# Kernel tuning notes

Hardware: AMD Instinct MI355X
Metric: run time of the kernel (lower is better)

The kernel has to match this reference:

```python
import jax, jax.numpy as jnp
import numpy as np

N = 100000       # num nodes
E = 3200000      # num edges (avg degree 32)
F_IN = 128       # num_node_features
HID = 16         # hidden dim hard-coded in Net
C = 10           # num_classes


def setup_inputs() -> dict:
    key = jax.random.key(0)
    k1, k2, k3, k4 = jax.random.split(key, 4)
    x = jax.random.normal(k1, (N, F_IN), dtype=jnp.float32)
    edge_index = jax.random.randint(k2, (2, E), 0, N, dtype=jnp.int32)
    W1 = jax.random.normal(k3, (F_IN, HID), dtype=jnp.float32) * 0.05
    b1 = jnp.zeros((HID,), dtype=jnp.float32)
    W2 = jax.random.normal(k4, (HID, C), dtype=jnp.float32) * 0.05
    b2 = jnp.zeros((C,), dtype=jnp.float32)
    return {"x": x, "edge_index": edge_index, "W1": W1, "b1": b1, "W2": W2, "b2": b2}


def reference(x, edge_index, W1, b1, W2, b2):
    # GCNConv: out = D^{-1/2} (A + I) D^{-1/2} X W + b   (add self-loops)
    loops = jnp.arange(N, dtype=edge_index.dtype)
    row = jnp.concatenate([edge_index[0], loops])  # source nodes
    col = jnp.concatenate([edge_index[1], loops])  # target nodes

    # symmetric normalization (degrees include self-loops, so deg >= 1)
    deg = jax.ops.segment_sum(jnp.ones_like(col, dtype=jnp.float32), col, num_segments=N)
    dis = jax.lax.rsqrt(deg)
    norm = dis[row] * dis[col]  # [E+N]

    def gcn_conv(h, W, b):
        h = h @ W                               # [N, d_out] small GEMM first
        msg = h[row] * norm[:, None]            # gather + scale, [E+N, d_out]
        out = jax.ops.segment_sum(msg, col, num_segments=N)  # scatter-add
        return out + b

    h = jax.nn.relu(gcn_conv(x, W1, b1))
    # F.dropout(training=False) is identity in eval mode
    logits = gcn_conv(h, W2, b2)
    return jax.nn.log_softmax(logits, axis=1)
```

## Files before the change

kernel.cpp:

```cpp
#include <hip/hip_runtime.h>
#include <math.h>

#define N_NODES 100000
#define N_EDGES 3200000
#define F_IN 128
#define HID 16
#define C_OUT 10
#define WIN 256
#define NDIG 391
#define PNB2 500
#define EPB 6400
#define SCN (NDIG * PNB2)
#define SB1 764
#define MAXE 40

typedef unsigned short u16;
typedef unsigned int u32;

__device__ __forceinline__ float bf2f(u16 u) {
    return __uint_as_float(((u32)u) << 16);
}
__device__ __forceinline__ u16 f2bf(float f) {
    u32 x = __float_as_uint(f);
    u32 r = (x + 0x7fffu + ((x >> 16) & 1u)) >> 16;
    return (u16)r;
}
__device__ __forceinline__ void acc8(float* a, uint4 w) {
    a[0] += bf2f((u16)(w.x & 0xffff)); a[1] += bf2f((u16)(w.x >> 16));
    a[2] += bf2f((u16)(w.y & 0xffff)); a[3] += bf2f((u16)(w.y >> 16));
    a[4] += bf2f((u16)(w.z & 0xffff)); a[5] += bf2f((u16)(w.z >> 16));
    a[6] += bf2f((u16)(w.w & 0xffff)); a[7] += bf2f((u16)(w.w >> 16));
}

__global__ void k_pcnt(const int* __restrict__ col, int* __restrict__ blkhistA) {
    __shared__ int h[NDIG];
    for (int i = threadIdx.x; i < NDIG; i += 256) h[i] = 0;
    __syncthreads();
    const uint4* c4 = (const uint4*)(col + blockIdx.x * EPB);
    for (int i = threadIdx.x; i < EPB / 4; i += 256) {
        uint4 c = c4[i];
        atomicAdd(&h[c.x >> 8], 1);
        atomicAdd(&h[c.y >> 8], 1);
        atomicAdd(&h[c.z >> 8], 1);
        atomicAdd(&h[c.w >> 8], 1);
    }
    __syncthreads();
    for (int d = threadIdx.x; d < NDIG; d += 256)
        blkhistA[d * PNB2 + blockIdx.x] = h[d];
}

__global__ void k_s1(const int* __restrict__ blkhistA, int* __restrict__ psum) {
    __shared__ int sm[256];
    int i = blockIdx.x * 256 + threadIdx.x;
    sm[threadIdx.x] = (i < SCN) ? blkhistA[i] : 0;
    __syncthreads();
    for (int off = 128; off > 0; off >>= 1) {
        if (threadIdx.x < off) sm[threadIdx.x] += sm[threadIdx.x + off];
        __syncthreads();
    }
    if (threadIdx.x == 0) psum[blockIdx.x] = sm[0];
}

__global__ void k_s2(int* __restrict__ psum) {
    const int T = 1024;
    __shared__ int part[T];
    int t = threadIdx.x;
    int v0 = (t < SB1) ? psum[t] : 0;
    part[t] = v0;
    __syncthreads();
    for (int off = 1; off < T; off <<= 1) {
        int v = part[t];
        int u = (t >= off) ? part[t - off] : 0;
        __syncthreads();
        part[t] = v + u;
        __syncthreads();
    }
    if (t < SB1) psum[t] = part[t] - v0;
}

__global__ void k_s3(const int* __restrict__ blkhistA, const int* __restrict__ psum,
                     int* __restrict__ blkhistB) {
    __shared__ int sm[256];
    int i = blockIdx.x * 256 + threadIdx.x;
    int t = threadIdx.x;
    int v = (i < SCN) ? blkhistA[i] : 0;
    sm[t] = v;
    __syncthreads();
    for (int off = 1; off < 256; off <<= 1) {
        int a = sm[t];
        int b = (t >= off) ? sm[t - off] : 0;
        __syncthreads();
        sm[t] = a + b;
        __syncthreads();
    }
    if (i < SCN) blkhistB[i] = psum[blockIdx.x] + sm[t] - v;
}

__global__ void __launch_bounds__(512) k_pwrite(
        const int* __restrict__ row, const int* __restrict__ col,
        const int* __restrict__ blkhistA, const int* __restrict__ blkhistB,
        u32* __restrict__ staging) {
    __shared__ u32 sorted[EPB];
    __shared__ u16 dwin[EPB];
    __shared__ int gbase[NDIG];
    __shared__ int lbase[NDIG];
    __shared__ int lcur[NDIG];
    __shared__ int scan[512];

    int t = threadIdx.x;
    int b = blockIdx.x;
    int hv = 0;
    if (t < NDIG) {
        hv = blkhistA[t * PNB2 + b];
        gbase[t] = blkhistB[t * PNB2 + b];
        lcur[t] = 0;
    }
    scan[t] = hv;
    __syncthreads();
    for (int off = 1; off < 512; off <<= 1) {
        int v = scan[t];
        int u = (t >= off) ? scan[t - off] : 0;
        __syncthreads();
        scan[t] = v + u;
        __syncthreads();
    }
    if (t < NDIG) lbase[t] = scan[t] - hv;
    __syncthreads();

    const uint4* c4 = (const uint4*)(col + b * EPB);
    const uint4* r4 = (const uint4*)(row + b * EPB);
    for (int i = t; i < EPB / 4; i += 512) {
        uint4 c = c4[i];
        uint4 r = r4[i];
        int d, rank, pos;
        d = (int)(c.x >> 8); rank = atomicAdd(&lcur[d], 1); pos = lbase[d] + rank;
        sorted[pos] = ((c.x & 255u) << 17) | r.x; dwin[pos] = (u16)d;
        d = (int)(c.y >> 8); rank = atomicAdd(&lcur[d], 1); pos = lbase[d] + rank;
        sorted[pos] = ((c.y & 255u) << 17) | r.y; dwin[pos] = (u16)d;
        d = (int)(c.z >> 8); rank = atomicAdd(&lcur[d], 1); pos = lbase[d] + rank;
        sorted[pos] = ((c.z & 255u) << 17) | r.z; dwin[pos] = (u16)d;
        d = (int)(c.w >> 8); rank = atomicAdd(&lcur[d], 1); pos = lbase[d] + rank;
        sorted[pos] = ((c.w & 255u) << 17) | r.w; dwin[pos] = (u16)d;
    }
    __syncthreads();

    for (int i = t; i < EPB; i += 512) {
        int d = dwin[i];
        staging[gbase[d] + (i - lbase[d])] = sorted[i];
    }
}

__global__ void k_csr(u32* staging, const int* __restrict__ blkhistB,
                      int* __restrict__ offs, float* __restrict__ dis) {
    __shared__ int cnt[WIN];
    __shared__ int base[WIN];
    int w = blockIdx.x;
    int t = threadIdx.x;
    cnt[t] = 0;
    __syncthreads();
    int start = blkhistB[w * PNB2];
    int end = (w == NDIG - 1) ? N_EDGES : blkhistB[(w + 1) * PNB2];
    u32 buf[MAXE];
    int n = 0;
#pragma unroll
    for (int k = 0; k < MAXE; k++) {
        int i = start + k * 256 + t;
        if (i < end) {
            u32 e = staging[i];
            buf[k] = e;
            n = k + 1;
            atomicAdd(&cnt[e >> 17], 1);
        }
    }
    __syncthreads();
    base[t] = cnt[t];
    __syncthreads();
    for (int off = 1; off < WIN; off <<= 1) {
        int v = base[t];
        int u = (t >= off) ? base[t - off] : 0;
        __syncthreads();
        base[t] = v + u;
        __syncthreads();
    }
    int excl = base[t] - cnt[t];
    base[t] = excl;
    int node = w * WIN + t;
    if (node < N_NODES) {
        offs[node] = start + excl;
        dis[node] = rsqrtf(1.0f + (float)cnt[t]);
    }
    if (w == 0 && t == 0) offs[N_NODES] = N_EDGES;
    __syncthreads();
    cnt[t] = 0;
    __syncthreads();
#pragma unroll
    for (int k = 0; k < MAXE; k++) {
        if (k < n) {
            u32 e = buf[k];
            int cl = (int)(e >> 17);
            int rank = atomicAdd(&cnt[cl], 1);
            staging[start + base[cl] + rank] = e;
        }
    }
}

__global__ void k_gemm1(const float* __restrict__ x, const float* __restrict__ W1,
                        const float* __restrict__ dis, u16* __restrict__ h1s) {
    __shared__ float Ws[F_IN * HID];
    for (int t = threadIdx.x; t < F_IN * HID; t += blockDim.x) Ws[t] = W1[t];
    __syncthreads();

    int node = blockIdx.x * blockDim.x + threadIdx.x;
    if (node >= N_NODES) return;

    float acc[HID];
#pragma unroll
    for (int j = 0; j < HID; j++) acc[j] = 0.f;

    const float4* xr = (const float4*)(x + (size_t)node * F_IN);
#pragma unroll 2
    for (int k4 = 0; k4 < F_IN / 4; k4++) {
        float4 v = xr[k4];
        float xv[4] = {v.x, v.y, v.z, v.w};
#pragma unroll
        for (int kk = 0; kk < 4; kk++) {
            const float4* wr = (const float4*)(Ws + (k4 * 4 + kk) * HID);
            float4 w0 = wr[0], w1 = wr[1], w2 = wr[2], w3 = wr[3];
            float xs = xv[kk];
            acc[0]  += xs * w0.x; acc[1]  += xs * w0.y; acc[2]  += xs * w0.z; acc[3]  += xs * w0.w;
            acc[4]  += xs * w1.x; acc[5]  += xs * w1.y; acc[6]  += xs * w1.z; acc[7]  += xs * w1.w;
            acc[8]  += xs * w2.x; acc[9]  += xs * w2.y; acc[10] += xs * w2.z; acc[11] += xs * w2.w;
            acc[12] += xs * w3.x; acc[13] += xs * w3.y; acc[14] += xs * w3.z; acc[15] += xs * w3.w;
        }
    }

    float d = dis[node];
    u32 p[8];
#pragma unroll
    for (int i = 0; i < 8; i++)
        p[i] = (u32)f2bf(acc[2 * i] * d) | ((u32)f2bf(acc[2 * i + 1] * d) << 16);
    u32* dst = (u32*)(h1s + (size_t)node * HID);
#pragma unroll
    for (int i = 0; i < 8; i++) dst[i] = p[i];
}

__global__ void k_gather1(const int* __restrict__ offs, const u32* __restrict__ csr,
                          const float* __restrict__ dis, const u16* __restrict__ h1s,
                          u16* __restrict__ agg1) {
    int t = blockIdx.x * 256 + threadIdx.x;
    if (t >= N_NODES * 2) return;
    int node = t >> 1;
    int half = t & 1;
    const uint4* hb = (const uint4*)h1s;
    float a[8] = {0.f, 0.f, 0.f, 0.f, 0.f, 0.f, 0.f, 0.f};
    acc8(a, hb[(size_t)node * 2 + half]);
    int s0 = offs[node], s1 = offs[node + 1];
    int j = s0;
    for (; j < s1 && (j & 3); j++)
        acc8(a, hb[(size_t)(csr[j] & 0x1FFFFu) * 2 + half]);
    for (; j + 4 <= s1; j += 4) {
        uint4 ss = *(const uint4*)(csr + j);
        uint4 w0 = hb[(size_t)(ss.x & 0x1FFFFu) * 2 + half];
        uint4 w1 = hb[(size_t)(ss.y & 0x1FFFFu) * 2 + half];
        uint4 w2 = hb[(size_t)(ss.z & 0x1FFFFu) * 2 + half];
        uint4 w3 = hb[(size_t)(ss.w & 0x1FFFFu) * 2 + half];
        acc8(a, w0); acc8(a, w1); acc8(a, w2); acc8(a, w3);
    }
    for (; j < s1; j++)
        acc8(a, hb[(size_t)(csr[j] & 0x1FFFFu) * 2 + half]);
    float dc = dis[node];
    uint4 o;
    o.x = (u32)f2bf(a[0] * dc) | ((u32)f2bf(a[1] * dc) << 16);
    o.y = (u32)f2bf(a[2] * dc) | ((u32)f2bf(a[3] * dc) << 16);
    o.z = (u32)f2bf(a[4] * dc) | ((u32)f2bf(a[5] * dc) << 16);
    o.w = (u32)f2bf(a[6] * dc) | ((u32)f2bf(a[7] * dc) << 16);
    ((uint4*)agg1)[(size_t)node * 2 + half] = o;
}

__global__ void k_layer2(const u16* __restrict__ agg1, const float* __restrict__ b1,
                         const float* __restrict__ W2, const float* __restrict__ dis,
                         u16* __restrict__ h2s) {
    __shared__ float Ws[HID * C_OUT];
    __shared__ float b1s[HID];
    if (threadIdx.x < HID * C_OUT) Ws[threadIdx.x] = W2[threadIdx.x];
    if (threadIdx.x < HID) b1s[threadIdx.x] = b1[threadIdx.x];
    __syncthreads();

    int node = blockIdx.x * blockDim.x + threadIdx.x;
    if (node >= N_NODES) return;

    const uint4* ar = (const uint4*)(agg1 + (size_t)node * HID);
    uint4 q0 = ar[0], q1 = ar[1];
    u32 qs[8] = {q0.x, q0.y, q0.z, q0.w, q1.x, q1.y, q1.z, q1.w};

    float acc[C_OUT];
#pragma unroll
    for (int k = 0; k < C_OUT; k++) acc[k] = 0.f;

#pragma unroll
    for (int i = 0; i < 8; i++) {
        u32 q = qs[i];
        float v0 = bf2f((u16)(q & 0xffff));
        float v1 = bf2f((u16)(q >> 16));
        int j0 = 2 * i, j1 = 2 * i + 1;
        float h0 = fmaxf(v0 + b1s[j0], 0.f);
        float h1v = fmaxf(v1 + b1s[j1], 0.f);
#pragma unroll
        for (int k = 0; k < C_OUT; k++) acc[k] += h0 * Ws[j0 * C_OUT + k] + h1v * Ws[j1 * C_OUT + k];
    }

    float d = dis[node];
    u32 p[8];
#pragma unroll
    for (int i = 0; i < 5; i++)
        p[i] = (u32)f2bf(acc[2 * i] * d) | ((u32)f2bf(acc[2 * i + 1] * d) << 16);
    p[5] = 0; p[6] = 0; p[7] = 0;
    u32* dst = (u32*)(h2s + (size_t)node * HID);
#pragma unroll
    for (int i = 0; i < 8; i++) dst[i] = p[i];
}

__global__ void k_gather2(const int* __restrict__ offs, const u32* __restrict__ csr,
                          const float* __restrict__ dis, const u16* __restrict__ h2s,
                          const float* __restrict__ b2, float* __restrict__ out) {
    __shared__ float b2s[C_OUT];
    if (threadIdx.x < C_OUT) b2s[threadIdx.x] = b2[threadIdx.x];
    __syncthreads();

    int t = blockIdx.x * 256 + threadIdx.x;
    if (t >= N_NODES * 2) return;
    int node = t >> 1;
    int half = t & 1;
    const uint4* hb = (const uint4*)h2s;
    float a[8] = {0.f, 0.f, 0.f, 0.f, 0.f, 0.f, 0.f, 0.f};
    acc8(a, hb[(size_t)node * 2 + half]);
    int s0 = offs[node], s1 = offs[node + 1];
    int j = s0;
    for (; j < s1 && (j & 3); j++)
        acc8(a, hb[(size_t)(csr[j] & 0x1FFFFu) * 2 + half]);
    for (; j + 4 <= s1; j += 4) {
        uint4 ss = *(const uint4*)(csr + j);
        uint4 w0 = hb[(size_t)(ss.x & 0x1FFFFu) * 2 + half];
        uint4 w1 = hb[(size_t)(ss.y & 0x1FFFFu) * 2 + half];
        uint4 w2 = hb[(size_t)(ss.z & 0x1FFFFu) * 2 + half];
        uint4 w3 = hb[(size_t)(ss.w & 0x1FFFFu) * 2 + half];
        acc8(a, w0); acc8(a, w1); acc8(a, w2); acc8(a, w3);
    }
    for (; j < s1; j++)
        acc8(a, hb[(size_t)(csr[j] & 0x1FFFFu) * 2 + half]);

    float dc = dis[node];
    int nf = half ? 2 : 8;
    float lg[8];
    float m = -1e30f;
#pragma unroll
    for (int k = 0; k < 8; k++) {
        lg[k] = a[k] * dc + b2s[(half * 8 + k) % C_OUT];
        if (k < nf) m = fmaxf(m, lg[k]);
    }
    m = fmaxf(m, __shfl_xor(m, 1));
    float s = 0.f;
#pragma unroll
    for (int k = 0; k < 8; k++)
        if (k < nf) s += expf(lg[k] - m);
    s += __shfl_xor(s, 1);
    float ls = logf(s) + m;
    float* dst = out + (size_t)node * C_OUT + half * 8;
    if (half == 0) {
#pragma unroll
        for (int i = 0; i < 4; i++)
            *(float2*)(dst + 2 * i) = make_float2(lg[2 * i] - ls, lg[2 * i + 1] - ls);
    } else {
        *(float2*)dst = make_float2(lg[0] - ls, lg[1] - ls);
    }
}

extern "C" void kernel_launch(void* const* d_in, const int* in_sizes, int n_in,
                              void* d_out, int out_size, void* d_ws, size_t ws_size,
                              hipStream_t stream) {
    const float* x  = (const float*)d_in[0];
    const int*   ei = (const int*)d_in[1];
    const float* W1 = (const float*)d_in[2];
    const float* b1 = (const float*)d_in[3];
    const float* W2 = (const float*)d_in[4];
    const float* b2 = (const float*)d_in[5];
    float* out = (float*)d_out;

    const int* row = ei;
    const int* col = ei + N_EDGES;

    char* ws = (char*)d_ws;
    float* dis      = (float*)(ws);
    int*   offs     = (int*)(ws + 400000);
    int*   blkhistA = (int*)(ws + 800016);
    int*   blkhistB = (int*)(ws + 1582352);
    int*   psum     = (int*)(ws + 2364688);
    u32*   staging  = (u32*)(ws + 2367744);
    u16*   h1s      = (u16*)(ws + 15167744);
    u16*   h2s      = (u16*)(ws + 15167744);
    u16*   agg1     = (u16*)d_out;
    float* agg2     = out;

    const int B = 256;
    int gN  = (N_NODES + B - 1) / B;
    int gN2 = (N_NODES * 2 + B - 1) / B;

    k_pcnt  <<<PNB2, B, 0, stream>>>(col, blkhistA);
    k_s1    <<<SB1, B, 0, stream>>>(blkhistA, psum);
    k_s2    <<<1, 1024, 0, stream>>>(psum);
    k_s3    <<<SB1, B, 0, stream>>>(blkhistA, psum, blkhistB);
    k_pwrite<<<PNB2, 512, 0, stream>>>(row, col, blkhistA, blkhistB, staging);
    k_csr   <<<NDIG, B, 0, stream>>>(staging, blkhistB, offs, dis);
    k_gemm1 <<<gN, B, 0, stream>>>(x, W1, dis, h1s);
    k_gather1<<<gN2, B, 0, stream>>>(offs, staging, dis, h1s, agg1);
    k_layer2<<<gN, B, 0, stream>>>(agg1, b1, W2, dis, h2s);
    k_gather2<<<gN2, B, 0, stream>>>(offs, staging, dis, h2s, b2, agg2);
    (void)agg2;
}
```

Measured before the change: 243.8 us.

## Fuse layer-1 gather with layer-2 transform and fold block-sum scan into s3

Merges the layer-1 neighbor aggregation with the bias+ReLU+W2 projection by exchanging the two half-rows between lane pairs with shuffles, removing the agg1 round trip through global memory and one kernel launch. The separate single-block prefix scan over block sums is eliminated; each k_s3 block now redundantly rescans the 764 partial sums in shared memory. Node offset loads are split across the lane pair and exchanged with a shuffle. The redundant scan adds per-block work and h2s moves to a separate workspace region.

```diff
diff --git a/kernel.cpp b/kernel.cpp
--- a/kernel.cpp
+++ b/kernel.cpp
@@ -61,28 +61,28 @@
     if (threadIdx.x == 0) psum[blockIdx.x] = sm[0];
 }
 
-__global__ void k_s2(int* __restrict__ psum) {
-    const int T = 1024;
-    __shared__ int part[T];
-    int t = threadIdx.x;
-    int v0 = (t < SB1) ? psum[t] : 0;
-    part[t] = v0;
-    __syncthreads();
-    for (int off = 1; off < T; off <<= 1) {
-        int v = part[t];
-        int u = (t >= off) ? part[t - off] : 0;
-        __syncthreads();
-        part[t] = v + u;
-        __syncthreads();
-    }
-    if (t < SB1) psum[t] = part[t] - v0;
-}
-
 __global__ void k_s3(const int* __restrict__ blkhistA, const int* __restrict__ psum,
                      int* __restrict__ blkhistB) {
+    __shared__ int ps[1024];
     __shared__ int sm[256];
-    int i = blockIdx.x * 256 + threadIdx.x;
     int t = threadIdx.x;
+    for (int i = t; i < 1024; i += 256) ps[i] = (i < SB1) ? psum[i] : 0;
+    __syncthreads();
+    for (int off = 1; off < 1024; off <<= 1) {
+        int v[4];
+#pragma unroll
+        for (int j = 0; j < 4; j++) {
+            int idx = t + j * 256;
+            v[j] = ps[idx] + ((idx >= off) ? ps[idx - off] : 0);
+        }
+        __syncthreads();
+#pragma unroll
+        for (int j = 0; j < 4; j++) ps[t + j * 256] = v[j];
+        __syncthreads();
+    }
+    int bpre = (blockIdx.x > 0) ? ps[blockIdx.x - 1] : 0;
+
+    int i = blockIdx.x * 256 + t;
     int v = (i < SCN) ? blkhistA[i] : 0;
     sm[t] = v;
     __syncthreads();
@@ -93,7 +93,7 @@
         sm[t] = a + b;
         __syncthreads();
     }
-    if (i < SCN) blkhistB[i] = psum[blockIdx.x] + sm[t] - v;
+    if (i < SCN) blkhistB[i] = bpre + sm[t] - v;
 }
 
 __global__ void __launch_bounds__(512) k_pwrite(
@@ -244,9 +244,16 @@
     for (int i = 0; i < 8; i++) dst[i] = p[i];
 }
 
-__global__ void k_gather1(const int* __restrict__ offs, const u32* __restrict__ csr,
-                          const float* __restrict__ dis, const u16* __restrict__ h1s,
-                          u16* __restrict__ agg1) {
+__global__ void k_gl1(const int* __restrict__ offs, const u32* __restrict__ csr,
+                      const float* __restrict__ dis, const u16* __restrict__ h1s,
+                      const float* __restrict__ b1, const float* __restrict__ W2,
+                      u16* __restrict__ h2s) {
+    __shared__ float Ws[HID * C_OUT];
+    __shared__ float b1s[HID];
+    if (threadIdx.x < HID * C_OUT) Ws[threadIdx.x] = W2[threadIdx.x];
+    if (threadIdx.x < HID) b1s[threadIdx.x] = b1[threadIdx.x];
+    __syncthreads();
+
     int t = blockIdx.x * 256 + threadIdx.x;
     if (t >= N_NODES * 2) return;
     int node = t >> 1;
@@ -254,7 +261,10 @@
     const uint4* hb = (const uint4*)h1s;
     float a[8] = {0.f, 0.f, 0.f, 0.f, 0.f, 0.f, 0.f, 0.f};
     acc8(a, hb[(size_t)node * 2 + half]);
-    int s0 = offs[node], s1 = offs[node + 1];
+    int o = offs[node + half];
+    int oo = __shfl_xor(o, 1);
+    int s0 = half ? oo : o;
+    int s1 = half ? o : oo;
     int j = s0;
     for (; j < s1 && (j & 3); j++)
         acc8(a, hb[(size_t)(csr[j] & 0x1FFFFu) * 2 + half]);
@@ -268,56 +278,40 @@
     }
     for (; j < s1; j++)
         acc8(a, hb[(size_t)(csr[j] & 0x1FFFFu) * 2 + half]);
+
     float dc = dis[node];
-    uint4 o;
-    o.x = (u32)f2bf(a[0] * dc) | ((u32)f2bf(a[1] * dc) << 16);
-    o.y = (u32)f2bf(a[2] * dc) | ((u32)f2bf(a[3] * dc) << 16);
-    o.z = (u32)f2bf(a[4] * dc) | ((u32)f2bf(a[5] * dc) << 16);
-    o.w = (u32)f2bf(a[6] * dc) | ((u32)f2bf(a[7] * dc) << 16);
-    ((uint4*)agg1)[(size_t)node * 2 + half] = o;
-}
-
-__global__ void k_layer2(const u16* __restrict__ agg1, const float* __restrict__ b1,
-                         const float* __restrict__ W2, const float* __restrict__ dis,
-                         u16* __restrict__ h2s) {
-    __shared__ float Ws[HID * C_OUT];
-    __shared__ float b1s[HID];
-    if (threadIdx.x < HID * C_OUT) Ws[threadIdx.x] = W2[threadIdx.x];
-    if (threadIdx.x < HID) b1s[threadIdx.x] = b1[threadIdx.x];
-    __syncthreads();
-
-    int node = blockIdx.x * blockDim.x + threadIdx.x;
-    if (node >= N_NODES) return;
-
-    const uint4* ar = (const uint4*)(agg1 + (size_t)node * HID);
-    uint4 q0 = ar[0], q1 = ar[1];
-    u32 qs[8] = {q0.x, q0.y, q0.z, q0.w, q1.x, q1.y, q1.z, q1.w};
-
-    float acc[C_OUT];
-#pragma unroll
-    for (int k = 0; k < C_OUT; k++) acc[k] = 0.f;
-
-#pragma unroll
-    for (int i = 0; i < 8; i++) {
-        u32 q = qs[i];
-        float v0 = bf2f((u16)(q & 0xffff));
-        float v1 = bf2f((u16)(q >> 16));
-        int j0 = 2 * i, j1 = 2 * i + 1;
-        float h0 = fmaxf(v0 + b1s[j0], 0.f);
-        float h1v = fmaxf(v1 + b1s[j1], 0.f);
-#pragma unroll
-        for (int k = 0; k < C_OUT; k++) acc[k] += h0 * Ws[j0 * C_OUT + k] + h1v * Ws[j1 * C_OUT + k];
-    }
-
-    float d = dis[node];
-    u32 p[8];
-#pragma unroll
-    for (int i = 0; i < 5; i++)
-        p[i] = (u32)f2bf(acc[2 * i] * d) | ((u32)f2bf(acc[2 * i + 1] * d) << 16);
-    p[5] = 0; p[6] = 0; p[7] = 0;
-    u32* dst = (u32*)(h2s + (size_t)node * HID);
-#pragma unroll
-    for (int i = 0; i < 8; i++) dst[i] = p[i];
+    float own[8], oth[8];
+#pragma unroll
+    for (int k = 0; k < 8; k++) own[k] = a[k] * dc;
+#pragma unroll
+    for (int k = 0; k < 8; k++) oth[k] = __shfl_xor(own[k], 1);
+    float h[16];
+#pragma unroll
+    for (int k = 0; k < 8; k++) {
+        h[k]     = half ? oth[k] : own[k];
+        h[8 + k] = half ? own[k] : oth[k];
+    }
+#pragma unroll
+    for (int jj = 0; jj < 16; jj++) h[jj] = fmaxf(h[jj] + b1s[jj], 0.f);
+
+    int nf = half ? 2 : 8;
+    float outv[8];
+#pragma unroll
+    for (int k = 0; k < 8; k++) {
+        float s = 0.f;
+        if (k < nf) {
+            int kk = half * 8 + k;
+#pragma unroll
+            for (int jj = 0; jj < 16; jj++) s += h[jj] * Ws[jj * C_OUT + kk];
+        }
+        outv[k] = s * dc;
+    }
+    uint4 ov;
+    ov.x = (u32)f2bf(outv[0]) | ((u32)f2bf(outv[1]) << 16);
+    ov.y = half ? 0u : ((u32)f2bf(outv[2]) | ((u32)f2bf(outv[3]) << 16));
+    ov.z = half ? 0u : ((u32)f2bf(outv[4]) | ((u32)f2bf(outv[5]) << 16));
+    ov.w = half ? 0u : ((u32)f2bf(outv[6]) | ((u32)f2bf(outv[7]) << 16));
+    ((uint4*)h2s)[(size_t)node * 2 + half] = ov;
 }
 
 __global__ void k_gather2(const int* __restrict__ offs, const u32* __restrict__ csr,
@@ -334,7 +328,10 @@
     const uint4* hb = (const uint4*)h2s;
     float a[8] = {0.f, 0.f, 0.f, 0.f, 0.f, 0.f, 0.f, 0.f};
     acc8(a, hb[(size_t)node * 2 + half]);
-    int s0 = offs[node], s1 = offs[node + 1];
+    int o = offs[node + half];
+    int oo = __shfl_xor(o, 1);
+    int s0 = half ? oo : o;
+    int s1 = half ? o : oo;
     int j = s0;
     for (; j < s1 && (j & 3); j++)
         acc8(a, hb[(size_t)(csr[j] & 0x1FFFFu) * 2 + half]);
@@ -397,9 +394,7 @@
     int*   psum     = (int*)(ws + 2364688);
     u32*   staging  = (u32*)(ws + 2367744);
     u16*   h1s      = (u16*)(ws + 15167744);
-    u16*   h2s      = (u16*)(ws + 15167744);
-    u16*   agg1     = (u16*)d_out;
-    float* agg2     = out;
+    u16*   h2s      = (u16*)(ws + 18367744);
 
     const int B = 256;
     int gN  = (N_NODES + B - 1) / B;
@@ -407,13 +402,10 @@
 
     k_pcnt  <<<PNB2, B, 0, stream>>>(col, blkhistA);
     k_s1    <<<SB1, B, 0, stream>>>(blkhistA, psum);
-    k_s2    <<<1, 1024, 0, stream>>>(psum);
     k_s3    <<<SB1, B, 0, stream>>>(blkhistA, psum, blkhistB);
     k_pwrite<<<PNB2, 512, 0, stream>>>(row, col, blkhistA, blkhistB, staging);
     k_csr   <<<NDIG, B, 0, stream>>>(staging, blkhistB, offs, dis);
     k_gemm1 <<<gN, B, 0, stream>>>(x, W1, dis, h1s);
-    k_gather1<<<gN2, B, 0, stream>>>(offs, staging, dis, h1s, agg1);
-    k_layer2<<<gN, B, 0, stream>>>(agg1, b1, W2, dis, h2s);
-    k_gather2<<<gN2, B, 0, stream>>>(offs, staging, dis, h2s, b2, agg2);
-    (void)agg2;
-}
+    k_gl1   <<<gN2, B, 0, stream>>>(offs, staging, dis, h1s, b1, W2, h2s);
+    k_gather2<<<gN2, B, 0, stream>>>(offs, staging, dis, h2s, b2, out);
+}
```

New measurement: 237.3 us. 2.7% less time.
